# Kernel tuning notes

Hardware: AMD Instinct MI355X
Metric: run time of the kernel (lower is better)

The kernel has to match this reference:

```python
import jax, jax.numpy as jnp
import numpy as np

SCALE = 0.125          # feature stride 8
OUT = 7                # roi_align output size
SR = 2                 # sampling_ratio
BBW = (10.0, 10.0, 5.0, 5.0)   # torchvision BoxCoder weights
CLAMP = float(np.log(1000.0 / 16.0))
IMG_H, IMG_W = 800.0, 1088.0


def _bilinear(img, ys, xs):
    # img [C,H,W]; ys,xs [P] -> [C,P]
    C, H, W = img.shape
    y = jnp.clip(ys, 0.0, H - 1.0)
    x = jnp.clip(xs, 0.0, W - 1.0)
    y0 = jnp.floor(y); x0 = jnp.floor(x)
    y0i = y0.astype(jnp.int32); x0i = x0.astype(jnp.int32)
    y1i = jnp.minimum(y0i + 1, H - 1); x1i = jnp.minimum(x0i + 1, W - 1)
    ly = y - y0; lx = x - x0
    flat = img.reshape(C, H * W)
    g = lambda yi, xi: flat[:, yi * W + xi]
    return (g(y0i, x0i) * (1 - ly) * (1 - lx) + g(y0i, x1i) * (1 - ly) * lx
            + g(y1i, x0i) * ly * (1 - lx) + g(y1i, x1i) * ly * lx)


def _roi_align(features, boxes, roi_batch):
    # features [B,C,H,W], boxes [N,4] (image coords), roi_batch [N] -> [N,C,7,7]
    B, C, H, W = features.shape
    P = OUT * SR

    def one(b, box):
        x1, y1, x2, y2 = box[0] * SCALE, box[1] * SCALE, box[2] * SCALE, box[3] * SCALE
        rw = jnp.maximum(x2 - x1, 1.0)
        rh = jnp.maximum(y2 - y1, 1.0)
        bw = rw / OUT; bh = rh / OUT
        off = (jnp.arange(OUT)[:, None] + (jnp.arange(SR)[None, :] + 0.5) / SR).reshape(-1)  # [P]
        ys = y1 + off * bh
        xs = x1 + off * bw
        yy = jnp.repeat(ys, P)   # [P*P], y-major
        xx = jnp.tile(xs, P)
        v = _bilinear(features[b], yy, xx)                   # [C, P*P]
        return v.reshape(C, OUT, SR, OUT, SR).mean(axis=(2, 4))  # avg over samples

    return jax.vmap(one)(roi_batch, boxes)


def _decode(deltas, boxes):
    # deltas [N,K,4], boxes [N,4] -> [N,K,4]
    pw = boxes[:, 2] - boxes[:, 0]
    ph = boxes[:, 3] - boxes[:, 1]
    cx = boxes[:, 0] + 0.5 * pw
    cy = boxes[:, 1] + 0.5 * ph
    dx = deltas[..., 0] / BBW[0]; dy = deltas[..., 1] / BBW[1]
    dw = jnp.minimum(deltas[..., 2] / BBW[2], CLAMP)
    dh = jnp.minimum(deltas[..., 3] / BBW[3], CLAMP)
    pcx = dx * pw[:, None] + cx[:, None]
    pcy = dy * ph[:, None] + cy[:, None]
    pww = jnp.exp(dw) * pw[:, None]
    phh = jnp.exp(dh) * ph[:, None]
    out = jnp.stack([
        jnp.clip(pcx - 0.5 * pww, 0.0, IMG_W),
        jnp.clip(pcy - 0.5 * phh, 0.0, IMG_H),
        jnp.clip(pcx + 0.5 * pww, 0.0, IMG_W),
        jnp.clip(pcy + 0.5 * phh, 0.0, IMG_H),
    ], axis=-1)
    return out


def setup_inputs() -> dict:
    key = jax.random.key(0)
    ks = jax.random.split(key, 12)
    B, C, H, W, N, NC = 2, 256, 100, 136, 1000, 2
    features = jax.random.normal(ks[0], (B, C, H, W), jnp.float32)
    # valid proposal boxes in image coords
    cx = jax.random.uniform(ks[1], (N,)) * IMG_W
    cy = jax.random.uniform(ks[2], (N,)) * IMG_H
    bw = jax.random.uniform(ks[3], (N,)) * 240.0 + 16.0
    bh = jax.random.uniform(ks[4], (N,)) * 240.0 + 16.0
    x1 = jnp.clip(cx - 0.5 * bw, 0.0, IMG_W - 2.0)
    y1 = jnp.clip(cy - 0.5 * bh, 0.0, IMG_H - 2.0)
    x2 = jnp.clip(x1 + bw, x1 + 1.0, IMG_W - 1.0)
    y2 = jnp.clip(y1 + bh, y1 + 1.0, IMG_H - 1.0)
    boxes = jnp.stack([x1, y1, x2, y2], axis=-1).astype(jnp.float32)
    roi_batch = jax.random.randint(ks[5], (N,), 0, B, dtype=jnp.int32)
    D = C * OUT * OUT  # 12544
    HID = 1024
    s = 0.02
    fc1_w = jax.random.normal(ks[6], (D, HID), jnp.float32) * s
    fc1_b = jnp.zeros((HID,), jnp.float32)
    fc2_w = jax.random.normal(ks[7], (HID, HID), jnp.float32) * s
    fc2_b = jnp.zeros((HID,), jnp.float32)
    cls_w = jax.random.normal(ks[8], (HID, NC), jnp.float32) * s
    cls_b = jnp.zeros((NC,), jnp.float32)
    bbox_w = jax.random.normal(ks[9], (HID, NC * 4), jnp.float32) * s
    bbox_b = jnp.zeros((NC * 4,), jnp.float32)
    return {"features": features, "boxes": boxes, "roi_batch": roi_batch,
            "fc1_w": fc1_w, "fc1_b": fc1_b, "fc2_w": fc2_w, "fc2_b": fc2_b,
            "cls_w": cls_w, "cls_b": cls_b, "bbox_w": bbox_w, "bbox_b": bbox_b}


def reference(features, boxes, roi_batch, fc1_w, fc1_b, fc2_w, fc2_b, cls_w, cls_b, bbox_w, bbox_b):
    N = boxes.shape[0]
    feats = _roi_align(features, boxes, roi_batch).reshape(N, -1)  # [N, 12544]
    h = jax.nn.relu(feats @ fc1_w + fc1_b)                         # TwoMLPHead fc6
    h = jax.nn.relu(h @ fc2_w + fc2_b)                             # TwoMLPHead fc7
    scores = jax.nn.softmax(h @ cls_w + cls_b, axis=-1)            # [N, 2]
    deltas = (h @ bbox_w + bbox_b).reshape(N, -1, 4)               # [N, 2, 4]
    dec = _decode(deltas, boxes).reshape(N, -1)                    # [N, 8]
    return jnp.concatenate([dec, scores], axis=-1)                 # [N, 10]
```

## Files before the change

### kernel.cpp

```cpp
#include <hip/hip_runtime.h>
#include <hip/hip_bf16.h>

#define BF16 __hip_bfloat16

typedef __bf16 bf16x8 __attribute__((ext_vector_type(8)));
typedef float floatx4 __attribute__((ext_vector_type(4)));

typedef const __attribute__((address_space(1))) void GV;
typedef __attribute__((address_space(3))) void LV;
#define GLD16(gp, lp) __builtin_amdgcn_global_load_lds((GV*)(gp), (LV*)(lp), 16, 0, 0)

__global__ __launch_bounds__(256) void transpose_all(const float* __restrict__ features,
                                                     const float* __restrict__ fc1_w,
                                                     const float* __restrict__ fc2_w,
                                                     BF16* __restrict__ featT,
                                                     BF16* __restrict__ w1t,
                                                     BF16* __restrict__ w2t) {
    __shared__ float tile[64][33];
    int bid = blockIdx.x;
    const float* ip;
    BF16* op;
    int R, C, cx, cy;
    if (bid < 3400) {
        int z = bid / 1700, r = bid - z * 1700;
        cx = r % 425; cy = r / 425;
        R = 256; C = 13600;
        ip = features + (size_t)z * 256 * 13600;
        op = featT + (size_t)z * 256 * 13600;
    } else if (bid < 9672) {
        int r = bid - 3400;
        cx = r & 31; cy = r >> 5;
        R = 12544; C = 1024;
        ip = fc1_w; op = w1t;
    } else {
        int r = bid - 9672;
        cx = r & 31; cy = r >> 5;
        R = 1024; C = 1024;
        ip = fc2_w; op = w2t;
    }
    int tx = threadIdx.x & 31, ty = threadIdx.x >> 5;
    int r0 = cy << 6, c0 = cx << 5;
#pragma unroll
    for (int i = 0; i < 8; ++i)
        tile[ty + i * 8][tx] = ip[(size_t)(r0 + ty + i * 8) * C + c0 + tx];
    __syncthreads();
#pragma unroll
    for (int i = 0; i < 4; ++i) {
        int c = ty + i * 8;
        BF16 a = __float2bfloat16(tile[tx * 2][c]);
        BF16 b = __float2bfloat16(tile[tx * 2 + 1][c]);
        unsigned int pk = (unsigned int)*(unsigned short*)&a |
                          ((unsigned int)*(unsigned short*)&b << 16);
        *(unsigned int*)(op + (size_t)(c0 + c) * R + r0 + tx * 2) = pk;
    }
}

__global__ __launch_bounds__(256) void roi_align_k(const BF16* __restrict__ featT,
                                                   const float* __restrict__ boxes,
                                                   const int* __restrict__ roi_batch,
                                                   BF16* __restrict__ feats) {
    __shared__ __align__(16) int   s_off[196][4];
    __shared__ __align__(16) float s_w[196][4];
    __shared__ BF16 lbuf[12544];
    int roi = blockIdx.x;
    int t = threadIdx.x;
    BF16* orow = feats + (size_t)roi * 12544;
    if (roi >= 1000) {
        uint4* o4 = (uint4*)orow;
        uint4 z = {0u, 0u, 0u, 0u};
        for (int i = t; i < 1568; i += 256) o4[i] = z;
        return;
    }
    int b = roi_batch[roi];

    if (t < 196) {
        float x1 = boxes[roi * 4 + 0] * 0.125f;
        float y1 = boxes[roi * 4 + 1] * 0.125f;
        float x2 = boxes[roi * 4 + 2] * 0.125f;
        float y2 = boxes[roi * 4 + 3] * 0.125f;
        float bw = fmaxf(x2 - x1, 1.0f) * (1.0f / 7.0f);
        float bh = fmaxf(y2 - y1, 1.0f) * (1.0f / 7.0f);
        int cell = t >> 2, s = t & 3;
        int oy = cell / 7, ox = cell - oy * 7;
        int sy = s >> 1, sx = s & 1;
        float yc = y1 + ((float)oy + ((float)sy + 0.5f) * 0.5f) * bh;
        float xc = x1 + ((float)ox + ((float)sx + 0.5f) * 0.5f) * bw;
        yc = fminf(fmaxf(yc, 0.0f), 99.0f);
        xc = fminf(fmaxf(xc, 0.0f), 135.0f);
        float y0f = floorf(yc), x0f = floorf(xc);
        int y0 = (int)y0f, x0 = (int)x0f;
        int y1i = min(y0 + 1, 99), x1i = min(x0 + 1, 135);
        float ly = yc - y0f, lx = xc - x0f;
        s_w[t][0] = (1.0f - ly) * (1.0f - lx) * 0.25f;
        s_w[t][1] = (1.0f - ly) * lx * 0.25f;
        s_w[t][2] = ly * (1.0f - lx) * 0.25f;
        s_w[t][3] = ly * lx * 0.25f;
        s_off[t][0] = (y0 * 136 + x0) * 256;
        s_off[t][1] = (y0 * 136 + x1i) * 256;
        s_off[t][2] = (y1i * 136 + x0) * 256;
        s_off[t][3] = (y1i * 136 + x1i) * 256;
    }
    __syncthreads();

    int cb = t & 31, g = t >> 5;
    const BF16* fb = featT + (size_t)b * (100 * 136 * 256) + cb * 8;
    int chbase = cb * 8;
    for (int cell = g; cell < 49; cell += 8) {
        float a[8];
#pragma unroll
        for (int j = 0; j < 8; ++j) a[j] = 0.0f;
#pragma unroll
        for (int s = 0; s < 4; ++s) {
            int p = cell * 4 + s;
#pragma unroll
            for (int tap = 0; tap < 4; ++tap) {
                float w = s_w[p][tap];
                bf16x8 v = *(const bf16x8*)(fb + s_off[p][tap]);
#pragma unroll
                for (int j = 0; j < 8; ++j) a[j] += w * (float)v[j];
            }
        }
#pragma unroll
        for (int j = 0; j < 8; ++j)
            lbuf[(chbase + j) * 49 + cell] = __float2bfloat16(a[j]);
    }
    __syncthreads();
    uint4* o4 = (uint4*)orow;
    const uint4* l4 = (const uint4*)lbuf;
    for (int i = t; i < 1568; i += 256) o4[i] = l4[i];
}

#define STAGE_TILE(kbi, bj)                                                     \
    do {                                                                        \
        size_t ko_ = (size_t)(kbi) * 128;                                       \
        _Pragma("unroll")                                                       \
        for (int i_ = 0; i_ < 4; ++i_) {                                        \
            GLD16(gA + (size_t)(i_ * 8) * strideA + ko_,                        \
                  &lds[bj][0][lw + i_ * 1024]);                                 \
            GLD16(gB + (size_t)(i_ * 8) * strideA + ko_,                        \
                  &lds[bj][1][lw + i_ * 1024]);                                 \
        }                                                                       \
    } while (0)

__global__ __launch_bounds__(256) void gemm_splitk(const BF16* __restrict__ A,
                                                   const BF16* __restrict__ Bt,
                                                   float* __restrict__ P,
                                                   int K, int chunk) {
    __shared__ char lds[2][2][16384];
    int b = blockIdx.x;
    int L = (b & 7) * (gridDim.x >> 3) + (b >> 3);
    int tn = L & 7, tm = (L >> 3) & 7, s = L >> 6;

    int w = threadIdx.x >> 6, l = threadIdx.x & 63;
    int wm = w & 1, wn = w >> 1;
    int k0 = s * chunk;

    floatx4 acc[4][4];
#pragma unroll
    for (int i = 0; i < 4; ++i)
#pragma unroll
        for (int j = 0; j < 4; ++j) acc[i][j] = (floatx4){0.f, 0.f, 0.f, 0.f};

    const size_t strideA = (size_t)K * 2;
    int r8 = l >> 3;
    int g8 = (l & 7) ^ r8;
    const char* gA = (const char*)A + (size_t)(tm * 128 + w * 32 + r8) * strideA
                     + (size_t)k0 * 2 + (size_t)g8 * 16;
    const char* gB = (const char*)Bt + (size_t)(tn * 128 + w * 32 + r8) * strideA
                     + (size_t)k0 * 2 + (size_t)g8 * 16;
    int lw = w * 4096 + l * 16;

    int c = l & 15, q = l >> 4;
    int xa0 = ((0 * 4 + q) ^ (c & 7)) * 16;
    int xa1 = ((1 * 4 + q) ^ (c & 7)) * 16;
    int abase = (wm * 64 + c) * 128;
    int bbase = (wn * 64 + c) * 128;

    int nIter = chunk >> 6;

    STAGE_TILE(0, 0);

    for (int kb = 0; kb < nIter; ++kb) {
        int cur = kb & 1;
        if (kb + 1 < nIter) {
            STAGE_TILE(kb + 1, cur ^ 1);
            asm volatile("s_waitcnt vmcnt(8)" ::: "memory");
        } else {
            asm volatile("s_waitcnt vmcnt(0)" ::: "memory");
        }
        __builtin_amdgcn_sched_barrier(0);
        __builtin_amdgcn_s_barrier();
        __builtin_amdgcn_sched_barrier(0);

        const char* bufA = lds[cur][0];
        const char* bufB = lds[cur][1];
#pragma unroll
        for (int kk = 0; kk < 2; ++kk) {
            int xo = kk ? xa1 : xa0;
            bf16x8 af[4], bfr[4];
#pragma unroll
            for (int mi = 0; mi < 4; ++mi) af[mi] = *(const bf16x8*)(bufA + abase + mi * 2048 + xo);
#pragma unroll
            for (int ni = 0; ni < 4; ++ni) bfr[ni] = *(const bf16x8*)(bufB + bbase + ni * 2048 + xo);
#pragma unroll
            for (int mi = 0; mi < 4; ++mi)
#pragma unroll
                for (int ni = 0; ni < 4; ++ni)
                    acc[mi][ni] = __builtin_amdgcn_mfma_f32_16x16x32_bf16(af[mi], bfr[ni], acc[mi][ni], 0, 0, 0);
        }
        __builtin_amdgcn_sched_barrier(0);
        __builtin_amdgcn_s_barrier();
    }

    size_t base = (size_t)s << 20;
#pragma unroll
    for (int mi = 0; mi < 4; ++mi) {
        int rowG = tm * 128 + wm * 64 + mi * 16 + q * 4;
#pragma unroll
        for (int ni = 0; ni < 4; ++ni) {
            int colG = tn * 128 + wn * 64 + ni * 16 + c;
#pragma unroll
            for (int r = 0; r < 4; ++r)
                P[base + (size_t)(rowG + r) * 1024 + colG] = acc[mi][ni][r];
        }
    }
}

__global__ __launch_bounds__(256) void gemm_fc2(const BF16* __restrict__ A,
                                                const BF16* __restrict__ Bt,
                                                const float* __restrict__ bias,
                                                float* __restrict__ H) {
    __shared__ char lds[2][2][16384];
    int b = blockIdx.x;
    int L = (b & 7) * 8 + (b >> 3);
    int tn = L & 7, tm = L >> 3;

    int w = threadIdx.x >> 6, l = threadIdx.x & 63;
    int wm = w & 1, wn = w >> 1;

    floatx4 acc[4][4];
#pragma unroll
    for (int i = 0; i < 4; ++i)
#pragma unroll
        for (int j = 0; j < 4; ++j) acc[i][j] = (floatx4){0.f, 0.f, 0.f, 0.f};

    const size_t strideA = 2048;
    int r8 = l >> 3;
    int g8 = (l & 7) ^ r8;
    const char* gA = (const char*)A + (size_t)(tm * 128 + w * 32 + r8) * strideA
                     + (size_t)g8 * 16;
    const char* gB = (const char*)Bt + (size_t)(tn * 128 + w * 32 + r8) * strideA
                     + (size_t)g8 * 16;
    int lw = w * 4096 + l * 16;

    int c = l & 15, q = l >> 4;
    int xa0 = ((0 * 4 + q) ^ (c & 7)) * 16;
    int xa1 = ((1 * 4 + q) ^ (c & 7)) * 16;
    int abase = (wm * 64 + c) * 128;
    int bbase = (wn * 64 + c) * 128;

    const int nIter = 16;

    STAGE_TILE(0, 0);

    for (int kb = 0; kb < nIter; ++kb) {
        int cur = kb & 1;
        if (kb + 1 < nIter) {
            STAGE_TILE(kb + 1, cur ^ 1);
            asm volatile("s_waitcnt vmcnt(8)" ::: "memory");
        } else {
            asm volatile("s_waitcnt vmcnt(0)" ::: "memory");
        }
        __builtin_amdgcn_sched_barrier(0);
        __builtin_amdgcn_s_barrier();
        __builtin_amdgcn_sched_barrier(0);

        const char* bufA = lds[cur][0];
        const char* bufB = lds[cur][1];
#pragma unroll
        for (int kk = 0; kk < 2; ++kk) {
            int xo = kk ? xa1 : xa0;
            bf16x8 af[4], bfr[4];
#pragma unroll
            for (int mi = 0; mi < 4; ++mi) af[mi] = *(const bf16x8*)(bufA + abase + mi * 2048 + xo);
#pragma unroll
            for (int ni = 0; ni < 4; ++ni) bfr[ni] = *(const bf16x8*)(bufB + bbase + ni * 2048 + xo);
#pragma unroll
            for (int mi = 0; mi < 4; ++mi)
#pragma unroll
                for (int ni = 0; ni < 4; ++ni)
                    acc[mi][ni] = __builtin_amdgcn_mfma_f32_16x16x32_bf16(af[mi], bfr[ni], acc[mi][ni], 0, 0, 0);
        }
        __builtin_amdgcn_sched_barrier(0);
        __builtin_amdgcn_s_barrier();
    }

#pragma unroll
    for (int mi = 0; mi < 4; ++mi) {
        int rowG = tm * 128 + wm * 64 + mi * 16 + q * 4;
#pragma unroll
        for (int ni = 0; ni < 4; ++ni) {
            int colG = tn * 128 + wn * 64 + ni * 16 + c;
            float bv = bias[colG];
#pragma unroll
            for (int r = 0; r < 4; ++r)
                H[(size_t)(rowG + r) * 1024 + colG] = fmaxf(acc[mi][ni][r] + bv, 0.0f);
        }
    }
}

__global__ __launch_bounds__(256) void reduce_k(const float* __restrict__ P,
                                                const float* __restrict__ bias,
                                                BF16* __restrict__ out,
                                                int S) {
    int i = blockIdx.x * 256 + threadIdx.x;
    float a = bias[i & 1023];
    for (int s = 0; s < S; ++s) a += P[((size_t)s << 20) + i];
    a = fmaxf(a, 0.0f);
    out[i] = __float2bfloat16(a);
}

__global__ __launch_bounds__(256) void head_k(const float* __restrict__ H,
                                              const float* __restrict__ cls_w,
                                              const float* __restrict__ cls_b,
                                              const float* __restrict__ bbox_w,
                                              const float* __restrict__ bbox_b,
                                              const float* __restrict__ boxes,
                                              float* __restrict__ out) {
    __shared__ float red[4][10];
    int roi = blockIdx.x;
    int t = threadIdx.x, w = t >> 6, l = t & 63;
    int k4 = t * 4;

    floatx4 h = *(const floatx4*)(H + (size_t)roi * 1024 + k4);

    float acc[10];
#pragma unroll
    for (int j = 0; j < 10; ++j) acc[j] = 0.0f;
    floatx4 c0 = *(const floatx4*)(cls_w + k4 * 2);
    floatx4 c1 = *(const floatx4*)(cls_w + k4 * 2 + 4);
    acc[0] = h.x * c0.x + h.y * c0.z + h.z * c1.x + h.w * c1.z;
    acc[1] = h.x * c0.y + h.y * c0.w + h.z * c1.y + h.w * c1.w;
    const float* bw = bbox_w + k4 * 8;
#pragma unroll
    for (int kk = 0; kk < 4; ++kk) {
        float hv = (kk == 0) ? h.x : (kk == 1) ? h.y : (kk == 2) ? h.z : h.w;
        floatx4 b0 = *(const floatx4*)(bw + kk * 8);
        floatx4 b1 = *(const floatx4*)(bw + kk * 8 + 4);
        acc[2] += hv * b0.x; acc[3] += hv * b0.y; acc[4] += hv * b0.z; acc[5] += hv * b0.w;
        acc[6] += hv * b1.x; acc[7] += hv * b1.y; acc[8] += hv * b1.z; acc[9] += hv * b1.w;
    }
#pragma unroll
    for (int j = 0; j < 10; ++j) {
#pragma unroll
        for (int off = 32; off > 0; off >>= 1) acc[j] += __shfl_down(acc[j], off);
    }
    if (l == 0) {
#pragma unroll
        for (int j = 0; j < 10; ++j) red[w][j] = acc[j];
    }
    __syncthreads();
    if (t == 0) {
        float f[10];
#pragma unroll
        for (int j = 0; j < 10; ++j) f[j] = red[0][j] + red[1][j] + red[2][j] + red[3][j];
        float s0 = f[0] + cls_b[0], s1 = f[1] + cls_b[1];
        float m = fmaxf(s0, s1);
        float e0 = expf(s0 - m), e1 = expf(s1 - m);
        float inv = 1.0f / (e0 + e1);

        float bx1 = boxes[roi * 4 + 0], by1 = boxes[roi * 4 + 1];
        float bx2 = boxes[roi * 4 + 2], by2 = boxes[roi * 4 + 3];
        float pw = bx2 - bx1, ph = by2 - by1;
        float cx = bx1 + 0.5f * pw, cy = by1 + 0.5f * ph;
        const float CLAMPV = 4.135166556742356f;
        float* orow = out + roi * 10;
#pragma unroll
        for (int cl = 0; cl < 2; ++cl) {
            float dx = (f[2 + cl * 4 + 0] + bbox_b[cl * 4 + 0]) * 0.1f;
            float dy = (f[2 + cl * 4 + 1] + bbox_b[cl * 4 + 1]) * 0.1f;
            float dw = fminf((f[2 + cl * 4 + 2] + bbox_b[cl * 4 + 2]) * 0.2f, CLAMPV);
            float dh = fminf((f[2 + cl * 4 + 3] + bbox_b[cl * 4 + 3]) * 0.2f, CLAMPV);
            float pcx = dx * pw + cx, pcy = dy * ph + cy;
            float pww = expf(dw) * pw, phh = expf(dh) * ph;
            orow[cl * 4 + 0] = fminf(fmaxf(pcx - 0.5f * pww, 0.0f), 1088.0f);
            orow[cl * 4 + 1] = fminf(fmaxf(pcy - 0.5f * phh, 0.0f), 800.0f);
            orow[cl * 4 + 2] = fminf(fmaxf(pcx + 0.5f * pww, 0.0f), 1088.0f);
            orow[cl * 4 + 3] = fminf(fmaxf(pcy + 0.5f * phh, 0.0f), 800.0f);
        }
        orow[8] = e0 * inv;
        orow[9] = e1 * inv;
    }
}

extern "C" void kernel_launch(void* const* d_in, const int* in_sizes, int n_in,
                              void* d_out, int out_size, void* d_ws, size_t ws_size,
                              hipStream_t stream) {
    const float* features = (const float*)d_in[0];
    const float* boxes    = (const float*)d_in[1];
    const int*   roi_b    = (const int*)d_in[2];
    const float* fc1_w    = (const float*)d_in[3];
    const float* fc1_b    = (const float*)d_in[4];
    const float* fc2_w    = (const float*)d_in[5];
    const float* fc2_b    = (const float*)d_in[6];
    const float* cls_w    = (const float*)d_in[7];
    const float* cls_b    = (const float*)d_in[8];
    const float* bbox_w   = (const float*)d_in[9];
    const float* bbox_b   = (const float*)d_in[10];
    float* out = (float*)d_out;

    char* ws = (char*)d_ws;
    BF16* featT = (BF16*)(ws + 0);
    BF16* w1t   = (BF16*)(ws + 13926400);
    BF16* w2t   = (BF16*)(ws + 39616512);
    BF16* feats = (BF16*)(ws + 41713664);
    BF16* h1    = (BF16*)(ws + 67403776);
    float* P1   = (float*)(ws + 69500928);
    float* H2   = (float*)(ws + 0);

    int S1 = 7;

    transpose_all<<<10184, 256, 0, stream>>>(features, fc1_w, fc2_w, featT, w1t, w2t);

    roi_align_k<<<1024, 256, 0, stream>>>(featT, boxes, roi_b, feats);

    gemm_splitk<<<64 * S1, 256, 0, stream>>>(feats, w1t, P1, 12544, 12544 / S1);
    reduce_k<<<4096, 256, 0, stream>>>(P1, fc1_b, h1, S1);

    gemm_fc2<<<64, 256, 0, stream>>>(h1, w2t, fc2_b, H2);

    head_k<<<1000, 256, 0, stream>>>(H2, cls_w, cls_b, bbox_w, bbox_b, boxes, out);
}
```

Before: 210.3 us.

## Overlap weight transpose with ROI align in a single combined kernel

Splits the combined transpose kernel so that only the feature transpose runs before ROI align. The fc1/fc2 weight transpose blocks now run in the same launch as the ROI align blocks, sharing one shared-memory buffer, so the memory-bound weight conversion can overlap with the gather-heavy ROI align work. The aim is to shorten the serialized critical path. In exchange, the ROI blocks now share the GPU with many transpose blocks and must use the larger unified shared-memory allocation.

```diff
diff --git a/kernel.cpp b/kernel.cpp
--- a/kernel.cpp
+++ b/kernel.cpp
@@ -10,34 +10,16 @@
 typedef __attribute__((address_space(3))) void LV;
 #define GLD16(gp, lp) __builtin_amdgcn_global_load_lds((GV*)(gp), (LV*)(lp), 16, 0, 0)
 
-__global__ __launch_bounds__(256) void transpose_all(const float* __restrict__ features,
-                                                     const float* __restrict__ fc1_w,
-                                                     const float* __restrict__ fc2_w,
-                                                     BF16* __restrict__ featT,
-                                                     BF16* __restrict__ w1t,
-                                                     BF16* __restrict__ w2t) {
+__global__ __launch_bounds__(256) void t_feat(const float* __restrict__ features,
+                                              BF16* __restrict__ featT) {
     __shared__ float tile[64][33];
     int bid = blockIdx.x;
-    const float* ip;
-    BF16* op;
-    int R, C, cx, cy;
-    if (bid < 3400) {
-        int z = bid / 1700, r = bid - z * 1700;
-        cx = r % 425; cy = r / 425;
-        R = 256; C = 13600;
-        ip = features + (size_t)z * 256 * 13600;
-        op = featT + (size_t)z * 256 * 13600;
-    } else if (bid < 9672) {
-        int r = bid - 3400;
-        cx = r & 31; cy = r >> 5;
-        R = 12544; C = 1024;
-        ip = fc1_w; op = w1t;
-    } else {
-        int r = bid - 9672;
-        cx = r & 31; cy = r >> 5;
-        R = 1024; C = 1024;
-        ip = fc2_w; op = w2t;
-    }
+    int z = bid / 1700, r = bid - z * 1700;
+    int cx = r % 425, cy = r / 425;
+    const int R = 256, C = 13600;
+    const float* ip = features + (size_t)z * 256 * 13600;
+    BF16* op = featT + (size_t)z * 256 * 13600;
+
     int tx = threadIdx.x & 31, ty = threadIdx.x >> 5;
     int r0 = cy << 6, c0 = cx << 5;
 #pragma unroll
@@ -55,15 +37,57 @@
     }
 }
 
-__global__ __launch_bounds__(256) void roi_align_k(const BF16* __restrict__ featT,
-                                                   const float* __restrict__ boxes,
-                                                   const int* __restrict__ roi_batch,
-                                                   BF16* __restrict__ feats) {
-    __shared__ __align__(16) int   s_off[196][4];
-    __shared__ __align__(16) float s_w[196][4];
-    __shared__ BF16 lbuf[12544];
-    int roi = blockIdx.x;
+__global__ __launch_bounds__(256) void roi_and_wt(const BF16* __restrict__ featT,
+                                                  const float* __restrict__ boxes,
+                                                  const int* __restrict__ roi_batch,
+                                                  BF16* __restrict__ feats,
+                                                  const float* __restrict__ fc1_w,
+                                                  const float* __restrict__ fc2_w,
+                                                  BF16* __restrict__ w1t,
+                                                  BF16* __restrict__ w2t) {
+    __shared__ __align__(16) char smem[31360];
+    int bid = blockIdx.x;
     int t = threadIdx.x;
+
+    if (bid >= 1024) {
+        float (*tile)[33] = (float(*)[33])smem;
+        int r = bid - 1024;
+        const float* ip;
+        BF16* op;
+        int R, C, cx, cy;
+        if (r < 6272) {
+            cx = r & 31; cy = r >> 5;
+            R = 12544; C = 1024;
+            ip = fc1_w; op = w1t;
+        } else {
+            r -= 6272;
+            cx = r & 31; cy = r >> 5;
+            R = 1024; C = 1024;
+            ip = fc2_w; op = w2t;
+        }
+        int tx = t & 31, ty = t >> 5;
+        int r0 = cy << 6, c0 = cx << 5;
+#pragma unroll
+        for (int i = 0; i < 8; ++i)
+            tile[ty + i * 8][tx] = ip[(size_t)(r0 + ty + i * 8) * C + c0 + tx];
+        __syncthreads();
+#pragma unroll
+        for (int i = 0; i < 4; ++i) {
+            int c = ty + i * 8;
+            BF16 a = __float2bfloat16(tile[tx * 2][c]);
+            BF16 b = __float2bfloat16(tile[tx * 2 + 1][c]);
+            unsigned int pk = (unsigned int)*(unsigned short*)&a |
+                              ((unsigned int)*(unsigned short*)&b << 16);
+            *(unsigned int*)(op + (size_t)(c0 + c) * R + r0 + tx * 2) = pk;
+        }
+        return;
+    }
+
+    int   (*s_off)[4] = (int(*)[4])smem;
+    float (*s_w)[4]   = (float(*)[4])(smem + 3136);
+    BF16* lbuf        = (BF16*)(smem + 6272);
+
+    int roi = bid;
     BF16* orow = feats + (size_t)roi * 12544;
     if (roi >= 1000) {
         uint4* o4 = (uint4*)orow;
@@ -420,9 +444,10 @@
 
     int S1 = 7;
 
-    transpose_all<<<10184, 256, 0, stream>>>(features, fc1_w, fc2_w, featT, w1t, w2t);
-
-    roi_align_k<<<1024, 256, 0, stream>>>(featT, boxes, roi_b, feats);
+    t_feat<<<3400, 256, 0, stream>>>(features, featT);
+
+    roi_and_wt<<<7808, 256, 0, stream>>>(featT, boxes, roi_b, feats,
+                                         fc1_w, fc2_w, w1t, w2t);
 
     gemm_splitk<<<64 * S1, 256, 0, stream>>>(feats, w1t, P1, 12544, 12544 / S1);
     reduce_k<<<4096, 256, 0, stream>>>(P1, fc1_b, h1, S1);
```

Result: no change. 207.5 us (-1.3%).
